# Kernel tuning notes

Hardware: AMD Instinct MI355X
Metric: run time of the kernel (lower is better)

Reference implementation:

```python
import jax, jax.numpy as jnp
import numpy as np

BS, N, H = 16, 128, 256
L, F = 9, 48  # lat_embed_dim, frac_embed_dim = 6*frac_freq
IN_DIM = 2 * H + L + F


def setup_inputs() -> dict:
    key = jax.random.key(0)
    ks = jax.random.split(key, 7)
    node_embed = jax.random.normal(ks[0], (BS, N, H), dtype=jnp.float32)
    edge_embed = jax.random.normal(ks[1], (BS, N, N, F), dtype=jnp.float32)
    graph_embed = jax.random.normal(ks[2], (BS, L), dtype=jnp.float32)
    s1 = 1.0 / np.sqrt(IN_DIM)
    s2 = 1.0 / np.sqrt(H)
    W1 = jax.random.uniform(ks[3], (IN_DIM, H), jnp.float32, -s1, s1)
    b1 = jax.random.uniform(ks[4], (H,), jnp.float32, -s1, s1)
    W2 = jax.random.uniform(ks[5], (H, H), jnp.float32, -s2, s2)
    b2 = jax.random.uniform(ks[6], (H,), jnp.float32, -s2, s2)
    return {"node_embed": node_embed, "edge_embed": edge_embed,
            "graph_embed": graph_embed, "W1": W1, "b1": b1, "W2": W2, "b2": b2}


def reference(node_embed, edge_embed, graph_embed, W1, b1, W2, b2):
    bs, n, h = node_embed.shape
    # Concat order matches torch: [node_j, node_i, graph, edge_ij]
    # First linear is applied to the concat; split W1 by segment so we never
    # materialize the (bs, N, N, 2H+L+F) concat tensor (same math).
    Wj = W1[:h]            # acts on node_embed[b, j]
    Wi = W1[h:2 * h]       # acts on node_embed[b, i]
    Wg = W1[2 * h:2 * h + L]  # acts on graph_embed[b]
    We = W1[2 * h + L:]    # acts on edge_embed[b, i, j]
    pj = node_embed @ Wj                      # (bs, N, H) -> broadcast over i
    pi = node_embed @ Wi                      # (bs, N, H) -> broadcast over j
    pg = graph_embed @ Wg                     # (bs, H)
    pe = jnp.einsum('bijf,fh->bijh', edge_embed, We)  # (bs, N, N, H)
    z1 = pe + pj[:, None, :, :] + pi[:, :, None, :] + pg[:, None, None, :] + b1
    h1 = jax.nn.silu(z1)
    edge_msg = jax.nn.silu(h1 @ W2 + b2)      # (bs, N, N, H)
    node_msg = edge_msg.mean(axis=2)          # mean over j
    return node_msg
```

## Files before the change

### kernel.cpp

```cpp
#include <hip/hip_runtime.h>

#define BSZ 16
#define NN  128
#define HH  256
#define LLG 9
#define FFE 48

typedef float        f32x4 __attribute__((ext_vector_type(4)));
typedef _Float16     f16x8 __attribute__((ext_vector_type(8)));
typedef unsigned int u32x4 __attribute__((ext_vector_type(4)));

static __device__ __forceinline__ unsigned short f2h_bits(float x) {
    _Float16 h = (_Float16)x;
    return __builtin_bit_cast(unsigned short, h);
}

static __device__ __forceinline__ float fast_silu(float x) {
    float e = __builtin_amdgcn_exp2f(x * -1.44269504088896341f);
    return x * __builtin_amdgcn_rcpf(1.0f + e);
}

__global__ __launch_bounds__(256) void pre_w(
    const float* __restrict__ W1, const float* __restrict__ W2,
    const float* __restrict__ graph, const float* __restrict__ b1,
    unsigned short* __restrict__ W2T, unsigned short* __restrict__ WeT,
    unsigned short* __restrict__ W1jiT, float* __restrict__ pg)
{
    const int blk = blockIdx.x;
    const int t   = threadIdx.x;
    if (blk < 256) {
        int tid = blk * 256 + t;
        int ho = tid >> 8, k = tid & 255;
        W2T[(ho << 8) + k] = f2h_bits(W2[(k << 8) + ho]);
        if (tid < 256 * 64) {
            int h = tid >> 6, f = tid & 63;
            WeT[(h << 6) + f] = (f < FFE) ? f2h_bits(W1[(521 + f) * HH + h])
                                          : (unsigned short)0;
        }
    } else if (blk < 768) {
        int tid = (blk - 256) * 256 + t;
        int hp = tid >> 8, f = tid & 255;
        int src = (((hp >> 8) << 8) + f) * HH + (hp & 255);
        W1jiT[(hp << 8) + f] = f2h_bits(W1[src]);
    } else {
        int b = blk - 768;
        float acc = b1[t];
        #pragma unroll
        for (int l = 0; l < LLG; ++l)
            acc = fmaf(graph[b * LLG + l], W1[(2 * HH + l) * HH + t], acc);
        pg[(b << 8) + t] = acc;
    }
}

__global__ __launch_bounds__(256) void pre_pjbase_mfma(
    const float* __restrict__ node, const unsigned short* __restrict__ W1jiT,
    const float* __restrict__ pg,
    float* __restrict__ pj, float* __restrict__ base)
{
    __shared__ unsigned char nls[32 * 512];
    const int tid = threadIdx.x;
    const int w    = tid >> 6;
    const int lane = tid & 63;
    const int q    = lane >> 4;
    const int c    = lane & 15;
    const int b  = blockIdx.x >> 2;
    const int r0 = (blockIdx.x & 3) << 5;
    const unsigned ck = (unsigned)(c & 7) << 4;

    const float* nb = node + (((size_t)b << 7) + r0) * HH;
    #pragma unroll
    for (int p = 0; p < 8; ++p) {
        const int e4 = (p << 8) + tid;
        const int r  = e4 >> 6, f4 = e4 & 63;
        const f32x4 x = *reinterpret_cast<const f32x4*>(nb + (e4 << 2));
        unsigned int lo = __builtin_bit_cast(unsigned int,
                            __builtin_amdgcn_cvt_pkrtz(x[0], x[1]));
        unsigned int hi = __builtin_bit_cast(unsigned int,
                            __builtin_amdgcn_cvt_pkrtz(x[2], x[3]));
        const unsigned off = (unsigned)(r << 9) +
            (((unsigned)(f4 << 3)) ^ ((unsigned)(r & 7) << 4));
        *reinterpret_cast<uint2*>(&nls[off]) = make_uint2(lo, hi);
    }
    __syncthreads();

    const int wh = w << 7;
    f32x4 acc[8][2];
    #pragma unroll
    for (int mt = 0; mt < 8; ++mt)
        #pragma unroll
        for (int nt = 0; nt < 2; ++nt) acc[mt][nt] = f32x4{0.f, 0.f, 0.f, 0.f};

    #pragma unroll 2
    for (int kk = 0; kk < 8; ++kk) {
        const unsigned kb = (unsigned)((kk << 6) + (q << 4));
        f16x8 bfr[2];
        #pragma unroll
        for (int nt = 0; nt < 2; ++nt) {
            const int r = (nt << 4) + c;
            bfr[nt] = *reinterpret_cast<const f16x8*>(
                &nls[(unsigned)(r << 9) + (kb ^ ck)]);
        }
        #pragma unroll
        for (int mt = 0; mt < 8; ++mt) {
            const f16x8 af = *reinterpret_cast<const f16x8*>(
                W1jiT + ((wh + (mt << 4) + c) << 8) + (kk << 5) + (q << 3));
            #pragma unroll
            for (int nt = 0; nt < 2; ++nt)
                acc[mt][nt] = __builtin_amdgcn_mfma_f32_16x16x32_f16(
                    af, bfr[nt], acc[mt][nt], 0, 0, 0);
        }
    }

    if (w < 2) {
        #pragma unroll
        for (int mt = 0; mt < 8; ++mt) {
            const int hb = wh + (mt << 4) + (q << 2);
            #pragma unroll
            for (int nt = 0; nt < 2; ++nt) {
                const int r = r0 + (nt << 4) + c;
                *reinterpret_cast<f32x4*>(
                    pj + (((size_t)b << 7) + r) * HH + hb) = acc[mt][nt];
            }
        }
    } else {
        #pragma unroll
        for (int mt = 0; mt < 8; ++mt) {
            const int hb = wh - 256 + (mt << 4) + (q << 2);
            const f32x4 pgv = *reinterpret_cast<const f32x4*>(
                pg + (b << 8) + hb);
            #pragma unroll
            for (int nt = 0; nt < 2; ++nt) {
                const int r = r0 + (nt << 4) + c;
                *reinterpret_cast<f32x4*>(
                    base + (((size_t)b << 7) + r) * HH + hb) = acc[mt][nt] + pgv;
            }
        }
    }
}

__global__ __launch_bounds__(512, 4) void fused_msg(
    const float* __restrict__ edge, const float* __restrict__ pj,
    const float* __restrict__ base, const unsigned short* __restrict__ W2T,
    const unsigned short* __restrict__ WeT, const float* __restrict__ b2,
    float* __restrict__ out)
{
    __shared__ unsigned char h1s[NN * HH * 2];
    __shared__ unsigned char efs[NN * 64 * 2];
    const int tid  = threadIdx.x;
    const int w    = tid >> 6;
    const int lane = tid & 63;
    const int q    = lane >> 4;
    const int c    = lane & 15;
    const int g    = blockIdx.x;
    const int bi   = ((g & 7) << 8) + (g >> 3);
    const int b    = bi >> 7;

    const float* eb = edge + (size_t)bi * (NN * FFE);

    #pragma unroll
    for (int p = 0; p < 3; ++p) {
        const int e4 = p * 512 + tid;
        const int j  = e4 / 12;
        const int f4 = e4 - j * 12;
        const f32x4 x = *reinterpret_cast<const f32x4*>(eb + (e4 << 2));
        unsigned int lo = __builtin_bit_cast(unsigned int,
                            __builtin_amdgcn_cvt_pkrtz(x[0], x[1]));
        unsigned int hi = __builtin_bit_cast(unsigned int,
                            __builtin_amdgcn_cvt_pkrtz(x[2], x[3]));
        const unsigned int off = (unsigned)(j << 7) +
            (((unsigned)(f4 << 3)) ^ ((unsigned)(j & 7) << 4));
        *reinterpret_cast<uint2*>(&efs[off]) = make_uint2(lo, hi);
    }
    {
        const int j = tid >> 2, gg = tid & 3;
        const unsigned int off = (unsigned)(j << 7) +
            (((unsigned)(96 + (gg << 3))) ^ ((unsigned)(j & 7) << 4));
        *reinterpret_cast<uint2*>(&efs[off]) = make_uint2(0u, 0u);
    }
    __syncthreads();

    f32x4 acc1[2][8];
    #pragma unroll
    for (int mt = 0; mt < 2; ++mt)
        #pragma unroll
        for (int nt = 0; nt < 8; ++nt) acc1[mt][nt] = f32x4{0.f, 0.f, 0.f, 0.f};

    #pragma unroll
    for (int kk = 0; kk < 2; ++kk) {
        const int koff = (kk << 5) + (q << 3);
        const int fb   = koff << 1;
        f16x8 af[2];
        #pragma unroll
        for (int mt = 0; mt < 2; ++mt) {
            const int row = (w << 5) + (mt << 4) + c;
            af[mt] = *reinterpret_cast<const f16x8*>(WeT + (row << 6) + koff);
        }
        #pragma unroll
        for (int nt = 0; nt < 8; ++nt) {
            const int j = (nt << 4) + c;
            const f16x8 bf = *reinterpret_cast<const f16x8*>(
                &efs[(unsigned)(j << 7) +
                     (((unsigned)fb) ^ ((unsigned)(j & 7) << 4))]);
            #pragma unroll
            for (int mt = 0; mt < 2; ++mt)
                acc1[mt][nt] = __builtin_amdgcn_mfma_f32_16x16x32_f16(
                    af[mt], bf, acc1[mt][nt], 0, 0, 0);
        }
    }

    #pragma unroll
    for (int mt = 0; mt < 2; ++mt) {
        const int h0 = (w << 5) + (mt << 4) + (q << 2);
        const f32x4 bb = *reinterpret_cast<const f32x4*>(
            base + ((size_t)bi << 8) + h0);
        #pragma unroll
        for (int nt = 0; nt < 8; ++nt) {
            const int jc = (nt << 4) + c;
            const f32x4 pjv = *reinterpret_cast<const f32x4*>(
                pj + (((size_t)b << 7) + jc) * HH + h0);
            float s0 = fast_silu(acc1[mt][nt][0] + bb[0] + pjv[0]);
            float s1 = fast_silu(acc1[mt][nt][1] + bb[1] + pjv[1]);
            float s2 = fast_silu(acc1[mt][nt][2] + bb[2] + pjv[2]);
            float s3 = fast_silu(acc1[mt][nt][3] + bb[3] + pjv[3]);
            unsigned int lo = __builtin_bit_cast(unsigned int,
                                __builtin_amdgcn_cvt_pkrtz(s0, s1));
            unsigned int hi = __builtin_bit_cast(unsigned int,
                                __builtin_amdgcn_cvt_pkrtz(s2, s3));
            const unsigned int off = (unsigned)(jc << 9) +
                (((unsigned)(h0 << 1)) ^ ((unsigned)(jc & 7) << 4));
            *reinterpret_cast<uint2*>(&h1s[off]) = make_uint2(lo, hi);
        }
    }
    __syncthreads();

    f32x4 acc2[8][2];
    #pragma unroll
    for (int mt = 0; mt < 8; ++mt)
        #pragma unroll
        for (int nt = 0; nt < 2; ++nt) acc2[mt][nt] = f32x4{0.f, 0.f, 0.f, 0.f};

    #pragma unroll 2
    for (int kk = 0; kk < 8; ++kk) {
        const int kb = (kk << 6) + (q << 4);
        f16x8 bw[2];
        #pragma unroll
        for (int nt = 0; nt < 2; ++nt) {
            const int ho = (w << 5) + (nt << 4) + c;
            bw[nt] = *reinterpret_cast<const f16x8*>(
                W2T + (ho << 8) + (kk << 5) + (q << 3));
        }
        #pragma unroll
        for (int gg = 0; gg < 2; ++gg) {
            f16x8 a2[4];
            #pragma unroll
            for (int m = 0; m < 4; ++m) {
                const int jc = ((gg << 2) + m) * 16 + c;
                const unsigned int off = (unsigned)(jc << 9) +
                    (((unsigned)kb) ^ ((unsigned)(jc & 7) << 4));
                a2[m] = *reinterpret_cast<const f16x8*>(&h1s[off]);
            }
            #pragma unroll
            for (int m = 0; m < 4; ++m)
                #pragma unroll
                for (int nt = 0; nt < 2; ++nt)
                    acc2[(gg << 2) + m][nt] = __builtin_amdgcn_mfma_f32_16x16x32_f16(
                        a2[m], bw[nt], acc2[(gg << 2) + m][nt], 0, 0, 0);
        }
    }

    float b2v[2];
    #pragma unroll
    for (int nt = 0; nt < 2; ++nt) b2v[nt] = b2[(w << 5) + (nt << 4) + c];

    float s[2] = {0.f, 0.f};
    #pragma unroll
    for (int nt = 0; nt < 2; ++nt)
        #pragma unroll
        for (int mt = 0; mt < 8; ++mt)
            #pragma unroll
            for (int r = 0; r < 4; ++r)
                s[nt] += fast_silu(acc2[mt][nt][r] + b2v[nt]);

    #pragma unroll
    for (int nt = 0; nt < 2; ++nt) {
        s[nt] += __shfl_xor(s[nt], 16);
        s[nt] += __shfl_xor(s[nt], 32);
    }
    if (q < 2)
        out[((size_t)bi << 8) + (w << 5) + (q << 4) + c] = s[q] * 0.0078125f;
}

extern "C" void kernel_launch(void* const* d_in, const int* in_sizes, int n_in,
                              void* d_out, int out_size, void* d_ws, size_t ws_size,
                              hipStream_t stream)
{
    const float* node  = (const float*)d_in[0];
    const float* edge  = (const float*)d_in[1];
    const float* graph = (const float*)d_in[2];
    const float* W1    = (const float*)d_in[3];
    const float* b1    = (const float*)d_in[4];
    const float* W2    = (const float*)d_in[5];
    const float* b2    = (const float*)d_in[6];
    float* out = (float*)d_out;

    char* ws = (char*)d_ws;
    unsigned short* W2T   = (unsigned short*)ws;
    unsigned short* WeT   = (unsigned short*)(ws + 131072);
    unsigned short* W1jiT = (unsigned short*)(ws + 163840);
    float* pg   = (float*)(ws + 425984);
    float* pj   = (float*)(ws + 442368);
    float* base = (float*)(ws + 442368 + 2097152);

    pre_w          <<<784, 256, 0, stream>>>(W1, W2, graph, b1, W2T, WeT, W1jiT, pg);
    pre_pjbase_mfma<<< 64, 256, 0, stream>>>(node, W1jiT, pg, pj, base);
    fused_msg      <<<BSZ * NN, 512, 0, stream>>>(edge, pj, base, W2T, WeT, b2, out);
}
```

Baseline: 100.1 us.

## Split fused_msg over two j-chunks to halve LDS and raise occupancy

The fused message kernel now handles the 128 j-neighbours in two chunks of 64. This halves the shared buffers for h1 and the staged edge features and cuts the accumulator register arrays, and launch bounds are raised from 4 to 6 blocks per CU. Staging of the second edge chunk is placed before the first chunk's second GEMM so the global load can overlap it. The cost is two extra barriers and reloading the W2 fragments for each chunk.

New measurement: 211.2 us. +111.0%, slower.

```diff
diff --git a/kernel.cpp b/kernel.cpp
--- a/kernel.cpp
+++ b/kernel.cpp
@@ -138,14 +138,14 @@
     }
 }
 
-__global__ __launch_bounds__(512, 4) void fused_msg(
+__global__ __launch_bounds__(512, 6) void fused_msg(
     const float* __restrict__ edge, const float* __restrict__ pj,
     const float* __restrict__ base, const unsigned short* __restrict__ W2T,
     const unsigned short* __restrict__ WeT, const float* __restrict__ b2,
     float* __restrict__ out)
 {
-    __shared__ unsigned char h1s[NN * HH * 2];
-    __shared__ unsigned char efs[NN * 64 * 2];
+    __shared__ unsigned char h1s[64 * HH * 2];
+    __shared__ unsigned char efs[64 * 64 * 2];
     const int tid  = threadIdx.x;
     const int w    = tid >> 6;
     const int lane = tid & 63;
@@ -157,12 +157,14 @@
 
     const float* eb = edge + (size_t)bi * (NN * FFE);
 
+    float b2v[2];
     #pragma unroll
-    for (int p = 0; p < 3; ++p) {
-        const int e4 = p * 512 + tid;
+    for (int nt = 0; nt < 2; ++nt) b2v[nt] = b2[(w << 5) + (nt << 4) + c];
+    float s[2] = {0.f, 0.f};
+
+    auto stage_write = [&](f32x4 x, int e4) {
         const int j  = e4 / 12;
         const int f4 = e4 - j * 12;
-        const f32x4 x = *reinterpret_cast<const f32x4*>(eb + (e4 << 2));
         unsigned int lo = __builtin_bit_cast(unsigned int,
                             __builtin_amdgcn_cvt_pkrtz(x[0], x[1]));
         unsigned int hi = __builtin_bit_cast(unsigned int,
@@ -170,116 +172,131 @@
         const unsigned int off = (unsigned)(j << 7) +
             (((unsigned)(f4 << 3)) ^ ((unsigned)(j & 7) << 4));
         *reinterpret_cast<uint2*>(&efs[off]) = make_uint2(lo, hi);
-    }
-    {
+    };
+    auto stage_chunk = [&](int chunk) {
+        const float* cb = eb + chunk * 3072;
+        f32x4 xa = *reinterpret_cast<const f32x4*>(cb + (tid << 2));
+        stage_write(xa, tid);
+        if (tid < 256) {
+            f32x4 xb = *reinterpret_cast<const f32x4*>(cb + ((512 + tid) << 2));
+            stage_write(xb, 512 + tid);
+        }
+    };
+
+    if (tid < 256) {
         const int j = tid >> 2, gg = tid & 3;
         const unsigned int off = (unsigned)(j << 7) +
             (((unsigned)(96 + (gg << 3))) ^ ((unsigned)(j & 7) << 4));
         *reinterpret_cast<uint2*>(&efs[off]) = make_uint2(0u, 0u);
     }
-    __syncthreads();
-
-    f32x4 acc1[2][8];
-    #pragma unroll
-    for (int mt = 0; mt < 2; ++mt)
-        #pragma unroll
-        for (int nt = 0; nt < 8; ++nt) acc1[mt][nt] = f32x4{0.f, 0.f, 0.f, 0.f};
-
-    #pragma unroll
-    for (int kk = 0; kk < 2; ++kk) {
-        const int koff = (kk << 5) + (q << 3);
-        const int fb   = koff << 1;
-        f16x8 af[2];
+
+    auto gemm1 = [&](int chunk) {
+        f32x4 acc1[2][4];
+        #pragma unroll
+        for (int mt = 0; mt < 2; ++mt)
+            #pragma unroll
+            for (int nt = 0; nt < 4; ++nt) acc1[mt][nt] = f32x4{0.f, 0.f, 0.f, 0.f};
+
+        #pragma unroll
+        for (int kk = 0; kk < 2; ++kk) {
+            const int koff = (kk << 5) + (q << 3);
+            const int fb   = koff << 1;
+            f16x8 af[2];
+            #pragma unroll
+            for (int mt = 0; mt < 2; ++mt) {
+                const int row = (w << 5) + (mt << 4) + c;
+                af[mt] = *reinterpret_cast<const f16x8*>(WeT + (row << 6) + koff);
+            }
+            #pragma unroll
+            for (int nt = 0; nt < 4; ++nt) {
+                const int j = (nt << 4) + c;
+                const f16x8 bf = *reinterpret_cast<const f16x8*>(
+                    &efs[(unsigned)(j << 7) +
+                         (((unsigned)fb) ^ ((unsigned)(j & 7) << 4))]);
+                #pragma unroll
+                for (int mt = 0; mt < 2; ++mt)
+                    acc1[mt][nt] = __builtin_amdgcn_mfma_f32_16x16x32_f16(
+                        af[mt], bf, acc1[mt][nt], 0, 0, 0);
+            }
+        }
+
         #pragma unroll
         for (int mt = 0; mt < 2; ++mt) {
-            const int row = (w << 5) + (mt << 4) + c;
-            af[mt] = *reinterpret_cast<const f16x8*>(WeT + (row << 6) + koff);
-        }
-        #pragma unroll
-        for (int nt = 0; nt < 8; ++nt) {
-            const int j = (nt << 4) + c;
-            const f16x8 bf = *reinterpret_cast<const f16x8*>(
-                &efs[(unsigned)(j << 7) +
-                     (((unsigned)fb) ^ ((unsigned)(j & 7) << 4))]);
-            #pragma unroll
-            for (int mt = 0; mt < 2; ++mt)
-                acc1[mt][nt] = __builtin_amdgcn_mfma_f32_16x16x32_f16(
-                    af[mt], bf, acc1[mt][nt], 0, 0, 0);
-        }
-    }
-
-    #pragma unroll
-    for (int mt = 0; mt < 2; ++mt) {
-        const int h0 = (w << 5) + (mt << 4) + (q << 2);
-        const f32x4 bb = *reinterpret_cast<const f32x4*>(
-            base + ((size_t)bi << 8) + h0);
-        #pragma unroll
-        for (int nt = 0; nt < 8; ++nt) {
-            const int jc = (nt << 4) + c;
-            const f32x4 pjv = *reinterpret_cast<const f32x4*>(
-                pj + (((size_t)b << 7) + jc) * HH + h0);
-            float s0 = fast_silu(acc1[mt][nt][0] + bb[0] + pjv[0]);
-            float s1 = fast_silu(acc1[mt][nt][1] + bb[1] + pjv[1]);
-            float s2 = fast_silu(acc1[mt][nt][2] + bb[2] + pjv[2]);
-            float s3 = fast_silu(acc1[mt][nt][3] + bb[3] + pjv[3]);
-            unsigned int lo = __builtin_bit_cast(unsigned int,
-                                __builtin_amdgcn_cvt_pkrtz(s0, s1));
-            unsigned int hi = __builtin_bit_cast(unsigned int,
-                                __builtin_amdgcn_cvt_pkrtz(s2, s3));
-            const unsigned int off = (unsigned)(jc << 9) +
-                (((unsigned)(h0 << 1)) ^ ((unsigned)(jc & 7) << 4));
-            *reinterpret_cast<uint2*>(&h1s[off]) = make_uint2(lo, hi);
-        }
-    }
-    __syncthreads();
-
-    f32x4 acc2[8][2];
-    #pragma unroll
-    for (int mt = 0; mt < 8; ++mt)
-        #pragma unroll
-        for (int nt = 0; nt < 2; ++nt) acc2[mt][nt] = f32x4{0.f, 0.f, 0.f, 0.f};
-
-    #pragma unroll 2
-    for (int kk = 0; kk < 8; ++kk) {
-        const int kb = (kk << 6) + (q << 4);
-        f16x8 bw[2];
-        #pragma unroll
-        for (int nt = 0; nt < 2; ++nt) {
-            const int ho = (w << 5) + (nt << 4) + c;
-            bw[nt] = *reinterpret_cast<const f16x8*>(
-                W2T + (ho << 8) + (kk << 5) + (q << 3));
-        }
-        #pragma unroll
-        for (int gg = 0; gg < 2; ++gg) {
+            const int h0 = (w << 5) + (mt << 4) + (q << 2);
+            const f32x4 bb = *reinterpret_cast<const f32x4*>(
+                base + ((size_t)bi << 8) + h0);
+            #pragma unroll
+            for (int nt = 0; nt < 4; ++nt) {
+                const int jc = (nt << 4) + c;
+                const int jg = (chunk << 6) + jc;
+                const f32x4 pjv = *reinterpret_cast<const f32x4*>(
+                    pj + (((size_t)b << 7) + jg) * HH + h0);
+                float s0 = fast_silu(acc1[mt][nt][0] + bb[0] + pjv[0]);
+                float s1 = fast_silu(acc1[mt][nt][1] + bb[1] + pjv[1]);
+                float s2 = fast_silu(acc1[mt][nt][2] + bb[2] + pjv[2]);
+                float s3 = fast_silu(acc1[mt][nt][3] + bb[3] + pjv[3]);
+                unsigned int lo = __builtin_bit_cast(unsigned int,
+                                    __builtin_amdgcn_cvt_pkrtz(s0, s1));
+                unsigned int hi = __builtin_bit_cast(unsigned int,
+                                    __builtin_amdgcn_cvt_pkrtz(s2, s3));
+                const unsigned int off = (unsigned)(jc << 9) +
+                    (((unsigned)(h0 << 1)) ^ ((unsigned)(jc & 7) << 4));
+                *reinterpret_cast<uint2*>(&h1s[off]) = make_uint2(lo, hi);
+            }
+        }
+    };
+
+    auto gemm2 = [&]() {
+        f32x4 acc2[4][2];
+        #pragma unroll
+        for (int m = 0; m < 4; ++m)
+            #pragma unroll
+            for (int nt = 0; nt < 2; ++nt) acc2[m][nt] = f32x4{0.f, 0.f, 0.f, 0.f};
+
+        const unsigned short* wp0 = W2T + (((w << 5) + c) << 8) + (q << 3);
+        const unsigned short* wp1 = wp0 + (16 << 8);
+
+        #pragma unroll 2
+        for (int kk = 0; kk < 8; ++kk) {
+            const f16x8 bw0 = *reinterpret_cast<const f16x8*>(wp0 + (kk << 5));
+            const f16x8 bw1 = *reinterpret_cast<const f16x8*>(wp1 + (kk << 5));
+            const int kb = (kk << 6) + (q << 4);
             f16x8 a2[4];
             #pragma unroll
             for (int m = 0; m < 4; ++m) {
-                const int jc = ((gg << 2) + m) * 16 + c;
+                const int jc = (m << 4) + c;
                 const unsigned int off = (unsigned)(jc << 9) +
                     (((unsigned)kb) ^ ((unsigned)(jc & 7) << 4));
                 a2[m] = *reinterpret_cast<const f16x8*>(&h1s[off]);
             }
             #pragma unroll
+            for (int m = 0; m < 4; ++m) {
+                acc2[m][0] = __builtin_amdgcn_mfma_f32_16x16x32_f16(
+                    a2[m], bw0, acc2[m][0], 0, 0, 0);
+                acc2[m][1] = __builtin_amdgcn_mfma_f32_16x16x32_f16(
+                    a2[m], bw1, acc2[m][1], 0, 0, 0);
+            }
+        }
+
+        #pragma unroll
+        for (int nt = 0; nt < 2; ++nt)
+            #pragma unroll
             for (int m = 0; m < 4; ++m)
                 #pragma unroll
-                for (int nt = 0; nt < 2; ++nt)
-                    acc2[(gg << 2) + m][nt] = __builtin_amdgcn_mfma_f32_16x16x32_f16(
-                        a2[m], bw[nt], acc2[(gg << 2) + m][nt], 0, 0, 0);
-        }
-    }
-
-    float b2v[2];
-    #pragma unroll
-    for (int nt = 0; nt < 2; ++nt) b2v[nt] = b2[(w << 5) + (nt << 4) + c];
-
-    float s[2] = {0.f, 0.f};
-    #pragma unroll
-    for (int nt = 0; nt < 2; ++nt)
-        #pragma unroll
-        for (int mt = 0; mt < 8; ++mt)
-            #pragma unroll
-            for (int r = 0; r < 4; ++r)
-                s[nt] += fast_silu(acc2[mt][nt][r] + b2v[nt]);
+                for (int r = 0; r < 4; ++r)
+                    s[nt] += fast_silu(acc2[m][nt][r] + b2v[nt]);
+    };
+
+    stage_chunk(0);
+    __syncthreads();
+    gemm1(0);
+    __syncthreads();
+    stage_chunk(1);
+    gemm2();
+    __syncthreads();
+    gemm1(1);
+    __syncthreads();
+    gemm2();
 
     #pragma unroll
     for (int nt = 0; nt < 2; ++nt) {
```
